# Kernel tuning notes

Hardware: AMD Instinct MI355X
Metric: run time of the kernel (lower is better)

## Reference

```python
import jax, jax.numpy as jnp
import numpy as np

N, E, D, L, H = 100000, 1600000, 64, 4, 4
C = D // H  # head dim = 16
NEG_SLOPE = 0.2


def layer_norm(x, g, b, eps=1e-5):
    m = jnp.mean(x, axis=-1, keepdims=True)
    v = jnp.var(x, axis=-1, keepdims=True)
    return (x - m) * jax.lax.rsqrt(v + eps) * g + b


def setup_inputs() -> dict:
    key = jax.random.key(0)
    ks = jax.random.split(key, 12)
    node_feats = jax.random.normal(ks[0], (N, D), jnp.float32)
    edge_feats = jax.random.normal(ks[1], (E, D), jnp.float32)
    edge_index = jax.random.randint(ks[2], (2, E), 0, N, jnp.int32)
    s = 0.1
    conv_w = jax.random.normal(ks[3], (L, D, H * C), jnp.float32) * s
    att_src = jax.random.normal(ks[4], (L, H, C), jnp.float32) * s
    att_dst = jax.random.normal(ks[5], (L, H, C), jnp.float32) * s
    edge_w = jax.random.normal(ks[6], (L, D, H * C), jnp.float32) * s
    att_edge = jax.random.normal(ks[7], (L, H, C), jnp.float32) * s
    conv_b = jnp.zeros((L, D), jnp.float32)
    ln_g = jnp.ones((L, D), jnp.float32)
    ln_b = jnp.zeros((L, D), jnp.float32)
    Din = 3 * D  # edge-update MLP input dim (node_i, node_j, edge)
    up1_w = jax.random.normal(ks[8], (L, Din, Din), jnp.float32) * 0.05
    up1_b = jnp.zeros((L, Din), jnp.float32)
    up_ln_g = jnp.ones((L, Din), jnp.float32)
    up_ln_b = jnp.zeros((L, Din), jnp.float32)
    up2_w = jax.random.normal(ks[9], (L, Din, D), jnp.float32) * 0.05
    up2_b = jnp.zeros((L, D), jnp.float32)
    return dict(node_feats=node_feats, edge_feats=edge_feats, edge_index=edge_index,
                conv_w=conv_w, att_src=att_src, att_dst=att_dst, edge_w=edge_w,
                att_edge=att_edge, conv_b=conv_b, ln_g=ln_g, ln_b=ln_b,
                up1_w=up1_w, up1_b=up1_b, up_ln_g=up_ln_g, up_ln_b=up_ln_b,
                up2_w=up2_w, up2_b=up2_b)


def _gat_conv(x, e, src, dst, w, a_s, a_d, ew, a_e, b):
    n = x.shape[0]
    # add self loops with zero edge attr
    loop = jnp.arange(n, dtype=src.dtype)
    src_f = jnp.concatenate([src, loop])
    dst_f = jnp.concatenate([dst, loop])
    xh = (x @ w).reshape(n, H, C)                       # [N,H,C]
    alpha_src = jnp.einsum('nhc,hc->nh', xh, a_s)        # [N,H]
    alpha_dst = jnp.einsum('nhc,hc->nh', xh, a_d)
    eh = (e @ ew).reshape(-1, H, C)                      # [E,H,C]
    alpha_edge = jnp.einsum('ehc,hc->eh', eh, a_e)       # [E,H]
    alpha_edge = jnp.concatenate([alpha_edge, jnp.zeros((n, H), x.dtype)])
    alpha = alpha_src[src_f] + alpha_dst[dst_f] + alpha_edge  # [E+N,H]
    alpha = jax.nn.leaky_relu(alpha, NEG_SLOPE)
    # segment softmax over destination neighborhoods
    amax = jax.ops.segment_max(alpha, dst_f, num_segments=n)
    alpha = jnp.exp(alpha - amax[dst_f])
    asum = jax.ops.segment_sum(alpha, dst_f, num_segments=n)
    alpha = alpha / (asum[dst_f] + 1e-16)
    msg = xh[src_f] * alpha[:, :, None]                  # [E+N,H,C]
    out = jax.ops.segment_sum(msg.reshape(-1, H * C), dst_f, num_segments=n)
    return out + b


def _edge_update(nf, ef, src, dst, w1, b1, g, bg, w2, b2):
    x = jnp.concatenate([nf[src], nf[dst], ef], axis=-1)  # [E,3D]
    h = layer_norm(x @ w1 + b1, g, bg)
    h = jax.nn.relu(h)
    return h @ w2 + b2 + ef


def reference(node_feats, edge_feats, edge_index, conv_w, att_src, att_dst,
              edge_w, att_edge, conv_b, ln_g, ln_b, up1_w, up1_b,
              up_ln_g, up_ln_b, up2_w, up2_b):
    src, dst = edge_index[0], edge_index[1]
    nf, ef = node_feats, edge_feats
    for l in range(L):
        conv = _gat_conv(nf, ef, src, dst, conv_w[l], att_src[l], att_dst[l],
                         edge_w[l], att_edge[l], conv_b[l])
        conv = layer_norm(conv, ln_g[l], ln_b[l])
        nf = jax.nn.relu(conv) + nf  # dropout in eval mode = identity
        ef = _edge_update(nf, ef, src, dst, up1_w[l], up1_b[l],
                          up_ln_g[l], up_ln_b[l], up2_w[l], up2_b[l])
    return nf, ef
```

## Files before the change

kernel.cpp:

```cpp
#include <hip/hip_runtime.h>
#include <math.h>

#define NN 100000
#define NE 1600000
#define DD 64
#define NL 4
#define NH 4
#define NC 16
#define DIN 192
#define SLOPE 0.2f
#define EB 64
#define XSTR 200
#define FSTR 66
#define RSTR 68
#define LOG2E 1.44269504088896340736f

typedef __bf16 bf8 __attribute__((ext_vector_type(8)));
typedef __bf16 bf4 __attribute__((ext_vector_type(4)));
typedef __bf16 bf2 __attribute__((ext_vector_type(2)));
typedef float f32x4 __attribute__((ext_vector_type(4)));

__device__ __forceinline__ f32x4 MFMA(bf8 a, bf8 b, f32x4 c) {
  return __builtin_amdgcn_mfma_f32_16x16x32_bf16(a, b, c, 0, 0, 0);
}

__global__ void k_prep(const float* __restrict__ up1_w, const float* __restrict__ up2_w,
                       const float* __restrict__ ew_all, const float* __restrict__ ae_all,
                       __bf16* __restrict__ W1H, __bf16* __restrict__ W2H,
                       float* __restrict__ vbuf, int* __restrict__ deg) {
  int bid = blockIdx.x;
  int tid = threadIdx.x;
  if (bid < 72) {
    int gidx = bid * 256 + tid;
    if (gidx >= 4 * 4608) return;
    int lyr = gidx / 4608, rem = gidx % 4608;
    int lane = rem & 63, ts = rem >> 6;
    int s = ts % 6, t = ts / 6;
    const float* Wl = up1_w + (size_t)lyr * DIN * DIN;
    size_t base = (size_t)lyr * 36864 + ((size_t)(t * 6 + s) * 64 + lane) * 8;
    int k0 = s * 32 + (lane >> 4) * 8, n = t * 16 + (lane & 15);
#pragma unroll
    for (int j = 0; j < 8; ++j)
      W1H[base + j] = (__bf16)Wl[(size_t)(k0 + j) * DIN + n];
  } else if (bid < 96) {
    int gidx = (bid - 72) * 256 + tid;
    if (gidx >= 4 * 1536) return;
    int lyr = gidx / 1536, rem = gidx % 1536;
    int lane = rem & 63, ts = rem >> 6;
    int s = ts % 6, t = ts / 6;
    const float* Wl = up2_w + (size_t)lyr * DIN * DD;
    size_t base = (size_t)lyr * 12288 + ((size_t)(t * 6 + s) * 64 + lane) * 8;
    int k0 = s * 32 + (lane >> 4) * 8, n = t * 16 + (lane & 15);
#pragma unroll
    for (int j = 0; j < 8; ++j)
      W2H[base + j] = (__bf16)Wl[(size_t)(k0 + j) * DD + n];
  } else if (bid < 100) {
    int l = bid - 96;
    const float* ew = ew_all + (size_t)l * DD * DD;
    const float* ae = ae_all + (size_t)l * NH * NC;
    int d = tid >> 2, h = tid & 3;
    float s = 0.f;
#pragma unroll
    for (int c = 0; c < NC; ++c) s = fmaf(ew[d * DD + h * NC + c], ae[h * NC + c], s);
    vbuf[l * 256 + d * NH + h] = s;
  } else {
    int i = (bid - 100) * 256 + tid;
    if (i < NN) deg[i] = 0;
  }
}

__global__ void k_w2v(const float* __restrict__ up2_w, const float* __restrict__ up2_b,
                      const float* __restrict__ vbuf, __bf16* __restrict__ W2VP,
                      __bf16* __restrict__ VP, float* __restrict__ bvdot) {
  int l = blockIdx.x;
  const float* vn = vbuf + (l + 1) * 256;
  int t = threadIdx.x;
  if (t < 384) {
    int s = t >> 6, lane = t & 63;
    int i = lane & 15, k0 = s * 32 + (lane >> 4) * 8;
    const float* W2 = up2_w + (size_t)l * DIN * DD;
    __bf16* out = W2VP + (size_t)l * 3072 + ((size_t)(s * 64 + lane)) * 8;
#pragma unroll
    for (int j = 0; j < 8; ++j) {
      float val = 0.f;
      if (i < 4)
        for (int n = 0; n < DD; ++n)
          val = fmaf(W2[(size_t)(k0 + j) * DD + n], vn[n * NH + i], val);
      out[j] = (__bf16)val;
    }
  }
  if (t < 128) {
    int s2 = t >> 6, lane = t & 63;
    int i = lane & 15, k0 = s2 * 32 + (lane >> 4) * 8;
    __bf16* out = VP + (size_t)l * 1024 + ((size_t)(s2 * 64 + lane)) * 8;
#pragma unroll
    for (int j = 0; j < 8; ++j)
      out[j] = (i < 4) ? (__bf16)vn[(k0 + j) * NH + i] : (__bf16)0.f;
  }
  if (t < 4) {
    const float* b2 = up2_b + (size_t)l * DD;
    float bv = 0.f;
    for (int n = 0; n < DD; ++n) bv = fmaf(b2[n], vn[n * NH + t], bv);
    bvdot[l * 4 + t] = bv;
  }
}

__global__ void k_hist(const int* __restrict__ dst, int* __restrict__ deg) {
  int e = blockIdx.x * 256 + threadIdx.x;
  if (e < NE) atomicAdd(&deg[dst[e]], 1);
}

__global__ void k_scan1(const int* __restrict__ deg, int* __restrict__ offs,
                        int* __restrict__ bsum) {
  __shared__ int sh[256];
  int t = threadIdx.x, b = blockIdx.x;
  int i0 = b * 1024 + t * 4;
  int d0 = (i0 + 0 < NN) ? deg[i0 + 0] : 0;
  int d1 = (i0 + 1 < NN) ? deg[i0 + 1] : 0;
  int d2 = (i0 + 2 < NN) ? deg[i0 + 2] : 0;
  int d3 = (i0 + 3 < NN) ? deg[i0 + 3] : 0;
  int s4 = d0 + d1 + d2 + d3;
  sh[t] = s4;
  __syncthreads();
  int p = 0;
#pragma unroll
  for (int off = 1; off < 256; off <<= 1) {
    int v = (t >= off) ? sh[t - off] : 0;
    __syncthreads();
    sh[t] += v;
    __syncthreads();
  }
  p = sh[t] - s4;
  if (t == 255) bsum[b] = sh[255];
  if (i0 + 0 < NN) offs[i0 + 0] = p;
  if (i0 + 1 < NN) offs[i0 + 1] = p + d0;
  if (i0 + 2 < NN) offs[i0 + 2] = p + d0 + d1;
  if (i0 + 3 < NN) offs[i0 + 3] = p + d0 + d1 + d2;
}

__global__ void k_scan2(int* __restrict__ bsum, int* __restrict__ boff,
                        int* __restrict__ offs, int nb) {
  if (threadIdx.x == 0 && blockIdx.x == 0) {
    int run = 0;
    for (int k = 0; k < nb; ++k) { boff[k] = run; run += bsum[k]; }
    offs[NN] = NE;
  }
}

__global__ void k_scan3(int* __restrict__ offs, const int* __restrict__ boff,
                        int* __restrict__ cursor) {
  int i = blockIdx.x * 256 + threadIdx.x;
  if (i < NN) {
    int v = offs[i] + boff[i >> 10];
    offs[i] = v;
    cursor[i] = v;
  }
}

__global__ void k_scatter(const int* __restrict__ src, const int* __restrict__ dst,
                          int* __restrict__ cursor, int2* __restrict__ csr_pack) {
  int e = blockIdx.x * 256 + threadIdx.x;
  if (e >= NE) return;
  int pos = atomicAdd(&cursor[dst[e]], 1);
  csr_pack[pos] = make_int2(src[e], e);
}

__global__ void k_xh0p1(const float* __restrict__ node_feats,
                        const float* __restrict__ edge_feats,
                        const float* __restrict__ W, const float* __restrict__ as_,
                        const float* __restrict__ ad_, const float* __restrict__ v,
                        __bf16* __restrict__ nf16, __bf16* __restrict__ xh16,
                        float* __restrict__ asrc, float* __restrict__ adst,
                        __bf16* __restrict__ ef16, float* __restrict__ araw) {
  int bid = blockIdx.x;
  if (bid < NN / 4 + 1) {
    int t = bid * 4 + (threadIdx.x >> 6);
    int d = threadIdx.x & 63;
    if (t >= NN) return;
    const float* x = node_feats + (size_t)t * DD;
    nf16[(size_t)t * DD + d] = (__bf16)x[d];
    float acc = 0.f;
#pragma unroll
    for (int k = 0; k < DD; ++k) acc = fmaf(x[k], W[k * DD + d], acc);
    xh16[(size_t)t * DD + d] = (__bf16)acc;
    int h = d >> 4, c = d & 15;
    float ps = acc * as_[h * NC + c];
    float pd = acc * ad_[h * NC + c];
#pragma unroll
    for (int off = 8; off >= 1; off >>= 1) {
      ps += __shfl_xor(ps, off, 64);
      pd += __shfl_xor(pd, off, 64);
    }
    if (c == 0) { asrc[t * NH + h] = ps; adst[t * NH + h] = pd; }
  } else {
    int e = (bid - (NN / 4 + 1)) * 64 + (threadIdx.x >> 2);
    int part = threadIdx.x & 3;
    if (e >= NE) return;
    float ph0 = 0.f, ph1 = 0.f, ph2 = 0.f, ph3 = 0.f;
    const float4* ep = (const float4*)(edge_feats + (size_t)e * DD + part * 16);
    const float4* v4 = (const float4*)v;
    bf4 outv[4];
#pragma unroll
    for (int c4 = 0; c4 < 4; ++c4) {
      float4 x = ep[c4];
      outv[c4][0] = (__bf16)x.x; outv[c4][1] = (__bf16)x.y;
      outv[c4][2] = (__bf16)x.z; outv[c4][3] = (__bf16)x.w;
      int d0 = part * 16 + c4 * 4;
      float4 va = v4[d0], vb = v4[d0 + 1], vc = v4[d0 + 2], vd = v4[d0 + 3];
      ph0 = fmaf(x.x, va.x, fmaf(x.y, vb.x, fmaf(x.z, vc.x, fmaf(x.w, vd.x, ph0))));
      ph1 = fmaf(x.x, va.y, fmaf(x.y, vb.y, fmaf(x.z, vc.y, fmaf(x.w, vd.y, ph1))));
      ph2 = fmaf(x.x, va.z, fmaf(x.y, vb.z, fmaf(x.z, vc.z, fmaf(x.w, vd.z, ph2))));
      ph3 = fmaf(x.x, va.w, fmaf(x.y, vb.w, fmaf(x.z, vc.w, fmaf(x.w, vd.w, ph3))));
    }
    *(bf8*)&ef16[(size_t)e * DD + part * 16] =
        (bf8){outv[0][0], outv[0][1], outv[0][2], outv[0][3],
              outv[1][0], outv[1][1], outv[1][2], outv[1][3]};
    *(bf8*)&ef16[(size_t)e * DD + part * 16 + 8] =
        (bf8){outv[2][0], outv[2][1], outv[2][2], outv[2][3],
              outv[3][0], outv[3][1], outv[3][2], outv[3][3]};
#pragma unroll
    for (int off = 1; off <= 2; off <<= 1) {
      ph0 += __shfl_xor(ph0, off, 64);
      ph1 += __shfl_xor(ph1, off, 64);
      ph2 += __shfl_xor(ph2, off, 64);
      ph3 += __shfl_xor(ph3, off, 64);
    }
    float pe = (part == 0) ? ph0 : (part == 1) ? ph1 : (part == 2) ? ph2 : ph3;
    araw[(size_t)e * NH + part] = pe;
  }
}

__global__ __launch_bounds__(256) void k_gather5(
    const __bf16* __restrict__ xh16, const float* __restrict__ araw,
    const int2* __restrict__ csr_pack, const int* __restrict__ offs,
    const float* __restrict__ asrc, const float* __restrict__ adst,
    const float* __restrict__ cb, const float* __restrict__ g,
    const float* __restrict__ bln, __bf16* __restrict__ nf16,
    float* __restrict__ nfout,
    const float* __restrict__ Wn, const float* __restrict__ asn,
    const float* __restrict__ adn, __bf16* __restrict__ xh16n,
    float* __restrict__ asrcn, float* __restrict__ adstn, int last) {
  int t = blockIdx.x * 4 + (threadIdx.x >> 6);
  int d = threadIdx.x & 63;
  if (t >= NN) return;
  int h = d >> 4;
  int o0 = offs[t], o1 = offs[t + 1];
  int deg = o1 - o0;
  float adh = adst[t * NH + h];

  float sh = asrc[t * NH + h] + adh;
  sh = ((sh > 0.f) ? sh : SLOPE * sh) * LOG2E;
  float m_run = sh;
  float wsum = 1.f;
  float acc = (float)xh16[(size_t)t * DD + d];

  int j = 0;
  for (; j + 3 < deg; j += 4) {
    int2 p0 = csr_pack[o0 + j], p1 = csr_pack[o0 + j + 1];
    int2 p2 = csr_pack[o0 + j + 2], p3 = csr_pack[o0 + j + 3];
    float ar0 = asrc[p0.x * NH + h] + adh + araw[(size_t)p0.y * NH + h];
    float ar1 = asrc[p1.x * NH + h] + adh + araw[(size_t)p1.y * NH + h];
    float ar2 = asrc[p2.x * NH + h] + adh + araw[(size_t)p2.y * NH + h];
    float ar3 = asrc[p3.x * NH + h] + adh + araw[(size_t)p3.y * NH + h];
    ar0 = ((ar0 > 0.f) ? ar0 : SLOPE * ar0) * LOG2E;
    ar1 = ((ar1 > 0.f) ? ar1 : SLOPE * ar1) * LOG2E;
    ar2 = ((ar2 > 0.f) ? ar2 : SLOPE * ar2) * LOG2E;
    ar3 = ((ar3 > 0.f) ? ar3 : SLOPE * ar3) * LOG2E;
    float x0 = (float)xh16[(size_t)p0.x * DD + d];
    float x1 = (float)xh16[(size_t)p1.x * DD + d];
    float x2 = (float)xh16[(size_t)p2.x * DD + d];
    float x3 = (float)xh16[(size_t)p3.x * DD + d];
    float mnew = fmaxf(fmaxf(m_run, fmaxf(ar0, ar1)), fmaxf(ar2, ar3));
    float rold = exp2f(m_run - mnew);
    float w0 = exp2f(ar0 - mnew), w1 = exp2f(ar1 - mnew);
    float w2 = exp2f(ar2 - mnew), w3 = exp2f(ar3 - mnew);
    acc = fmaf(w3, x3, fmaf(w2, x2, fmaf(w1, x1, fmaf(w0, x0, acc * rold))));
    wsum = (w0 + w1) + (w2 + w3) + wsum * rold;
    m_run = mnew;
  }
  for (; j < deg; ++j) {
    int2 p = csr_pack[o0 + j];
    float ar = asrc[p.x * NH + h] + adh + araw[(size_t)p.y * NH + h];
    ar = ((ar > 0.f) ? ar : SLOPE * ar) * LOG2E;
    float xv = (float)xh16[(size_t)p.x * DD + d];
    float mnew = fmaxf(m_run, ar);
    float rold = exp2f(m_run - mnew);
    float w = exp2f(ar - mnew);
    acc = fmaf(w, xv, acc * rold);
    wsum = fmaf(w, 1.f, wsum * rold);
    m_run = mnew;
  }

  float val = acc / (wsum + 1e-16f) + cb[d];
  float m = val;
#pragma unroll
  for (int off = 32; off >= 1; off >>= 1) m += __shfl_xor(m, off, 64);
  m *= (1.f / 64.f);
  float c = val - m;
  float q = c * c;
#pragma unroll
  for (int off = 32; off >= 1; off >>= 1) q += __shfl_xor(q, off, 64);
  float rstd = 1.f / sqrtf(q * (1.f / 64.f) + 1e-5f);
  float y = c * rstd * g[d] + bln[d];
  y = fmaxf(y, 0.f);
  float out = y + (float)nf16[(size_t)t * DD + d];
  nf16[(size_t)t * DD + d] = (__bf16)out;

  if (last) {
    nfout[(size_t)t * DD + d] = out;
  } else {
    float acc2 = 0.f;
#pragma unroll 8
    for (int k = 0; k < DD; ++k) {
      float xk = __shfl(out, k, 64);
      acc2 = fmaf(xk, Wn[k * DD + d], acc2);
    }
    xh16n[(size_t)t * DD + d] = (__bf16)acc2;
    int cc = d & 15;
    float ps = acc2 * asn[h * NC + cc];
    float pd = acc2 * adn[h * NC + cc];
#pragma unroll
    for (int off = 8; off >= 1; off >>= 1) {
      ps += __shfl_xor(ps, off, 64);
      pd += __shfl_xor(pd, off, 64);
    }
    if (cc == 0) { asrcn[t * NH + h] = ps; adstn[t * NH + h] = pd; }
  }
}

__global__ __launch_bounds__(256, 4) void k_edge_mlp16(
    const __bf16* __restrict__ nf16, __bf16* __restrict__ ef16,
    float* __restrict__ efout,
    const int* __restrict__ src, const int* __restrict__ dst,
    const __bf16* __restrict__ W1H, const float* __restrict__ b1,
    const float* __restrict__ g, const float* __restrict__ bg,
    const __bf16* __restrict__ W2H, const float* __restrict__ b2,
    const __bf16* __restrict__ W2VP, const __bf16* __restrict__ VP,
    const float* __restrict__ bvdot, float* __restrict__ araw, int last) {
  __shared__ __bf16 XH[EB * XSTR];
  __shared__ __bf16 RESB[EB * RSTR];
  __shared__ __bf16 Pb[EB * 8];
  int tid = threadIdx.x;
  int e0 = blockIdx.x * EB;
  float* XF = (float*)XH;

  {
    int row = tid >> 2, p = tid & 3;
    int se = src[e0 + row], de = dst[e0 + row];
    const bf8* psrc = (const bf8*)(nf16 + (size_t)se * DD + p * 16);
    *(bf8*)&XH[row * XSTR + p * 16]     = psrc[0];
    *(bf8*)&XH[row * XSTR + p * 16 + 8] = psrc[1];
    const bf8* pdst = (const bf8*)(nf16 + (size_t)de * DD + p * 16);
    *(bf8*)&XH[row * XSTR + 64 + p * 16]     = pdst[0];
    *(bf8*)&XH[row * XSTR + 64 + p * 16 + 8] = pdst[1];
    const bf8* pef = (const bf8*)(ef16 + (size_t)(e0 + row) * DD + p * 16);
    bf8 ev0 = pef[0], ev1 = pef[1];
    *(bf8*)&XH[row * XSTR + 128 + p * 16]     = ev0;
    *(bf8*)&XH[row * XSTR + 128 + p * 16 + 8] = ev1;
    *(bf8*)&RESB[row * RSTR + p * 16]     = ev0;
    *(bf8*)&RESB[row * RSTR + p * 16 + 8] = ev1;
  }
  __syncthreads();

  int cg = tid >> 6, l = tid & 63;
  int gq = l >> 4, i = l & 15;
  int col = cg * 16 + i;

  f32x4 acc[4][3];
#pragma unroll
  for (int rt = 0; rt < 4; ++rt)
#pragma unroll
    for (int t = 0; t < 3; ++t) acc[rt][t] = (f32x4){0.f, 0.f, 0.f, 0.f};
  f32x4 accQ = (f32x4){0.f, 0.f, 0.f, 0.f};

#pragma unroll
  for (int s = 0; s < 6; ++s) {
    bf8 a[4];
#pragma unroll
    for (int rt = 0; rt < 4; ++rt)
      a[rt] = *(const bf8*)&XH[(rt * 16 + i) * XSTR + s * 32 + gq * 8];
#pragma unroll
    for (int t = 0; t < 3; ++t) {
      bf8 bh = *(const bf8*)(W1H + ((size_t)((cg * 3 + t) * 6 + s) * 64 + l) * 8);
#pragma unroll
      for (int rt = 0; rt < 4; ++rt) acc[rt][t] = MFMA(a[rt], bh, acc[rt][t]);
    }
  }

  float b1v[3], gv[3], bgv[3];
#pragma unroll
  for (int t = 0; t < 3; ++t) {
    int n = cg * 48 + t * 16 + i;
    b1v[t] = b1[n]; gv[t] = g[n]; bgv[t] = bg[n];
  }
#pragma unroll
  for (int rt = 0; rt < 4; ++rt)
#pragma unroll
    for (int t = 0; t < 3; ++t)
#pragma unroll
      for (int r = 0; r < 4; ++r) acc[rt][t][r] += b1v[t];

#pragma unroll
  for (int rt = 0; rt < 4; ++rt)
#pragma unroll
    for (int r = 0; r < 4; ++r) {
      float sm = 0.f, sq = 0.f;
#pragma unroll
      for (int t = 0; t < 3; ++t) { float x = acc[rt][t][r]; sm += x; sq = fmaf(x, x, sq); }
#pragma unroll
      for (int off = 1; off <= 8; off <<= 1) {
        sm += __shfl_xor(sm, off, 64);
        sq += __shfl_xor(sq, off, 64);
      }
      if (i == 0) {
        int row = rt * 16 + gq * 4 + r;
        bf2 pr; pr[0] = (__bf16)sm; pr[1] = (__bf16)sq;
        *(bf2*)&Pb[row * 8 + cg * 2] = pr;
      }
    }
  __syncthreads();

  if (tid < EB) {
    bf8 pv = *(const bf8*)&Pb[tid * 8];
    float sm = (float)pv[0] + (float)pv[2] + (float)pv[4] + (float)pv[6];
    float sq = (float)pv[1] + (float)pv[3] + (float)pv[5] + (float)pv[7];
    float mean = sm * (1.f / (float)DIN);
    float var = sq * (1.f / (float)DIN) - mean * mean;
    float rstd = 1.f / sqrtf(var + 1e-5f);
    bf2 mv; mv[0] = (__bf16)mean; mv[1] = (__bf16)rstd;
    *(bf2*)&Pb[tid * 8] = mv;
  }
  __syncthreads();

#pragma unroll
  for (int rt = 0; rt < 4; ++rt)
#pragma unroll
    for (int r = 0; r < 4; ++r) {
      int row = rt * 16 + gq * 4 + r;
      bf2 mv = *(const bf2*)&Pb[row * 8];
      float mean = (float)mv[0], rstd = (float)mv[1];
#pragma unroll
      for (int t = 0; t < 3; ++t) {
        float y = (acc[rt][t][r] - mean) * rstd * gv[t] + bgv[t];
        y = fmaxf(y, 0.f);
        XH[row * XSTR + cg * 48 + t * 16 + i] = (__bf16)y;
      }
    }
  __syncthreads();

  f32x4 acc2[4];
#pragma unroll
  for (int rt = 0; rt < 4; ++rt) acc2[rt] = (f32x4){0.f, 0.f, 0.f, 0.f};

#pragma unroll
  for (int s = 0; s < 6; ++s) {
    bf8 a2[4];
#pragma unroll
    for (int rt = 0; rt < 4; ++rt)
      a2[rt] = *(const bf8*)&XH[(rt * 16 + i) * XSTR + s * 32 + gq * 8];
    bf8 bh = *(const bf8*)(W2H + ((size_t)(cg * 6 + s) * 64 + l) * 8);
#pragma unroll
    for (int rt = 0; rt < 4; ++rt) acc2[rt] = MFMA(a2[rt], bh, acc2[rt]);
    if (!last) {
      bf8 acg = *(const bf8*)&XH[(cg * 16 + i) * XSTR + s * 32 + gq * 8];
      bf8 wv = *(const bf8*)(W2VP + ((size_t)(s * 64 + l)) * 8);
      accQ = MFMA(acg, wv, accQ);
    }
  }
  if (!last) {
#pragma unroll
    for (int s2 = 0; s2 < 2; ++s2) {
      bf8 ae = *(const bf8*)&RESB[(cg * 16 + i) * RSTR + s2 * 32 + gq * 8];
      bf8 vp = *(const bf8*)(VP + ((size_t)(s2 * 64 + l)) * 8);
      accQ = MFMA(ae, vp, accQ);
    }
  }
  __syncthreads();

  float b2v = b2[col];
#pragma unroll
  for (int rt = 0; rt < 4; ++rt)
#pragma unroll
    for (int r = 0; r < 4; ++r) {
      int row = rt * 16 + gq * 4 + r;
      float resv = (float)RESB[row * RSTR + col];
      XF[row * FSTR + col] = acc2[rt][r] + b2v + resv;
    }

  if (!last && i < 4) {
    float bvd = bvdot[i];
#pragma unroll
    for (int r = 0; r < 4; ++r) {
      int row = cg * 16 + gq * 4 + r;
      araw[(size_t)(e0 + row) * NH + i] = accQ[r] + bvd;
    }
  }
  __syncthreads();

  {
    int row = tid >> 2, q = tid & 3;
    const float* fr = &XF[row * FSTR + q * 16];
    if (last) {
      float* op = efout + (size_t)(e0 + row) * DD + q * 16;
#pragma unroll
      for (int k = 0; k < 4; ++k)
        *(float4*)(op + k * 4) = *(const float4*)(fr + k * 4);
    } else {
      bf8 o0, o1;
#pragma unroll
      for (int k = 0; k < 8; ++k) { o0[k] = (__bf16)fr[k]; o1[k] = (__bf16)fr[k + 8]; }
      __bf16* op = ef16 + (size_t)(e0 + row) * DD + q * 16;
      *(bf8*)op = o0;
      *(bf8*)(op + 8) = o1;
    }
  }
}

extern "C" void kernel_launch(void* const* d_in, const int* in_sizes, int n_in,
                              void* d_out, int out_size, void* d_ws, size_t ws_size,
                              hipStream_t stream) {
  const float* node_feats = (const float*)d_in[0];
  const float* edge_feats = (const float*)d_in[1];
  const int*   edge_index = (const int*)d_in[2];
  const float* conv_w  = (const float*)d_in[3];
  const float* att_src = (const float*)d_in[4];
  const float* att_dst = (const float*)d_in[5];
  const float* edge_w  = (const float*)d_in[6];
  const float* att_edge= (const float*)d_in[7];
  const float* conv_b  = (const float*)d_in[8];
  const float* ln_g    = (const float*)d_in[9];
  const float* ln_b    = (const float*)d_in[10];
  const float* up1_w   = (const float*)d_in[11];
  const float* up1_b   = (const float*)d_in[12];
  const float* up_ln_g = (const float*)d_in[13];
  const float* up_ln_b = (const float*)d_in[14];
  const float* up2_w   = (const float*)d_in[15];
  const float* up2_b   = (const float*)d_in[16];

  const int* src = edge_index;
  const int* dst = edge_index + NE;

  float* nf = (float*)d_out;
  float* efout = nf + (size_t)NN * DD;

  float* w = (float*)d_ws;
  __bf16* xh16a = (__bf16*)w; w += (size_t)NN * DD / 2;
  __bf16* xh16b = (__bf16*)w; w += (size_t)NN * DD / 2;
  __bf16* nf16 = (__bf16*)w; w += (size_t)NN * DD / 2;
  __bf16* ef16 = (__bf16*)w; w += (size_t)NE * DD / 2;
  float* asA   = w; w += (size_t)NN * NH;
  float* adA   = w; w += (size_t)NN * NH;
  float* asB   = w; w += (size_t)NN * NH;
  float* adB   = w; w += (size_t)NN * NH;
  float* araw  = w; w += (size_t)NE * NH;
  float* vbuf  = w; w += 4 * 256;
  float* bvdot = w; w += 16;
  __bf16* W1H  = (__bf16*)w; w += (size_t)4 * 36864 / 2;
  __bf16* W2H  = (__bf16*)w; w += (size_t)4 * 12288 / 2;
  __bf16* W2VP = (__bf16*)w; w += (size_t)3 * 3072 / 2;
  __bf16* VPb  = (__bf16*)w; w += (size_t)3 * 1024 / 2;
  int* deg     = (int*)w; w += NN;
  int* offs    = (int*)w; w += NN + 2;
  int* cursor  = (int*)w; w += NN;
  int* bsum    = (int*)w; w += 128;
  int* boff    = (int*)w; w += 128;
  int2* csr_pack = (int2*)w; w += (size_t)NE * 2;

  __bf16* xh[2] = {xh16a, xh16b};
  float* as_[2] = {asA, asB};
  float* ad_[2] = {adA, adB};

  const int nb = (NN + 1023) / 1024;
  const int nzero = (NN + 255) / 256;

  k_prep<<<100 + nzero, 256, 0, stream>>>(up1_w, up2_w, edge_w, att_edge,
                                          W1H, W2H, vbuf, deg);
  k_hist<<<(NE + 255) / 256, 256, 0, stream>>>(dst, deg);
  k_scan1<<<nb, 256, 0, stream>>>(deg, offs, bsum);
  k_scan2<<<1, 64, 0, stream>>>(bsum, boff, offs, nb);
  k_scan3<<<(NN + 255) / 256, 256, 0, stream>>>(offs, boff, cursor);
  k_scatter<<<(NE + 255) / 256, 256, 0, stream>>>(src, dst, cursor, csr_pack);

  k_w2v<<<3, 384, 0, stream>>>(up2_w, up2_b, vbuf, W2VP, VPb, bvdot);
  k_xh0p1<<<(NN / 4 + 1) + NE / 64, 256, 0, stream>>>(
      node_feats, edge_feats, conv_w, att_src, att_dst, vbuf,
      nf16, xh16a, asA, adA, ef16, araw);

  for (int l = 0; l < NL; ++l) {
    int last = (l == NL - 1) ? 1 : 0;
    int cur = l & 1, nxt = (l + 1) & 1;
    k_gather5<<<NN / 4 + 1, 256, 0, stream>>>(
        xh[cur], araw, csr_pack, offs, as_[cur], ad_[cur],
        conv_b + (size_t)l * DD, ln_g + (size_t)l * DD, ln_b + (size_t)l * DD,
        nf16, nf,
        last ? conv_w : (conv_w + (size_t)(l + 1) * DD * DD),
        last ? att_src : (att_src + (size_t)(l + 1) * NH * NC),
        last ? att_dst : (att_dst + (size_t)(l + 1) * NH * NC),
        xh[nxt], as_[nxt], ad_[nxt], last);
    k_edge_mlp16<<<NE / EB, 256, 0, stream>>>(
        nf16, ef16, efout, src, dst,
        W1H + (size_t)l * 36864, up1_b + (size_t)l * DIN,
        up_ln_g + (size_t)l * DIN, up_ln_b + (size_t)l * DIN,
        W2H + (size_t)l * 12288, up2_b + (size_t)l * DD,
        last ? W2VP : (W2VP + (size_t)l * 3072),
        last ? VPb : (VPb + (size_t)l * 1024),
        bvdot + (size_t)l * 4, araw, last);
  }
}
```

Before: 2.524 ms.

## Store edge features and attention logits in CSR (dst-sorted) order

Edge-indexed intermediates (ef16, araw) are now stored in CSR position order instead of original edge order. The gather kernel then reads araw contiguously instead of through a random edge-id indirection. The edge MLP processes edges in dst-sorted order, so destination node reads hit cache better, and it scatters back to the original edge index only on the final-layer fp32 output. The cost is an extra csr_dst array, a permuted first read of edge_feats, and a scattered final write.

Result: no change. 2.486 ms (-1.5%).

```diff
diff --git a/kernel.cpp b/kernel.cpp
--- a/kernel.cpp
+++ b/kernel.cpp
@@ -158,17 +158,21 @@
 }
 
 __global__ void k_scatter(const int* __restrict__ src, const int* __restrict__ dst,
-                          int* __restrict__ cursor, int2* __restrict__ csr_pack) {
+                          int* __restrict__ cursor, int2* __restrict__ csr_pack,
+                          int* __restrict__ csr_dst) {
   int e = blockIdx.x * 256 + threadIdx.x;
   if (e >= NE) return;
-  int pos = atomicAdd(&cursor[dst[e]], 1);
+  int de = dst[e];
+  int pos = atomicAdd(&cursor[de], 1);
   csr_pack[pos] = make_int2(src[e], e);
+  csr_dst[pos] = de;
 }
 
 __global__ void k_xh0p1(const float* __restrict__ node_feats,
                         const float* __restrict__ edge_feats,
                         const float* __restrict__ W, const float* __restrict__ as_,
                         const float* __restrict__ ad_, const float* __restrict__ v,
+                        const int2* __restrict__ csr_pack,
                         __bf16* __restrict__ nf16, __bf16* __restrict__ xh16,
                         float* __restrict__ asrc, float* __restrict__ adst,
                         __bf16* __restrict__ ef16, float* __restrict__ araw) {
@@ -193,9 +197,10 @@
     }
     if (c == 0) { asrc[t * NH + h] = ps; adst[t * NH + h] = pd; }
   } else {
-    int e = (bid - (NN / 4 + 1)) * 64 + (threadIdx.x >> 2);
+    int pos = (bid - (NN / 4 + 1)) * 64 + (threadIdx.x >> 2);
     int part = threadIdx.x & 3;
-    if (e >= NE) return;
+    if (pos >= NE) return;
+    int e = csr_pack[pos].y;
     float ph0 = 0.f, ph1 = 0.f, ph2 = 0.f, ph3 = 0.f;
     const float4* ep = (const float4*)(edge_feats + (size_t)e * DD + part * 16);
     const float4* v4 = (const float4*)v;
@@ -212,10 +217,10 @@
       ph2 = fmaf(x.x, va.z, fmaf(x.y, vb.z, fmaf(x.z, vc.z, fmaf(x.w, vd.z, ph2))));
       ph3 = fmaf(x.x, va.w, fmaf(x.y, vb.w, fmaf(x.z, vc.w, fmaf(x.w, vd.w, ph3))));
     }
-    *(bf8*)&ef16[(size_t)e * DD + part * 16] =
+    *(bf8*)&ef16[(size_t)pos * DD + part * 16] =
         (bf8){outv[0][0], outv[0][1], outv[0][2], outv[0][3],
               outv[1][0], outv[1][1], outv[1][2], outv[1][3]};
-    *(bf8*)&ef16[(size_t)e * DD + part * 16 + 8] =
+    *(bf8*)&ef16[(size_t)pos * DD + part * 16 + 8] =
         (bf8){outv[2][0], outv[2][1], outv[2][2], outv[2][3],
               outv[3][0], outv[3][1], outv[3][2], outv[3][3]};
 #pragma unroll
@@ -226,11 +231,11 @@
       ph3 += __shfl_xor(ph3, off, 64);
     }
     float pe = (part == 0) ? ph0 : (part == 1) ? ph1 : (part == 2) ? ph2 : ph3;
-    araw[(size_t)e * NH + part] = pe;
-  }
-}
-
-__global__ __launch_bounds__(256) void k_gather5(
+    araw[(size_t)pos * NH + part] = pe;
+  }
+}
+
+__global__ __launch_bounds__(256) void k_gather7(
     const __bf16* __restrict__ xh16, const float* __restrict__ araw,
     const int2* __restrict__ csr_pack, const int* __restrict__ offs,
     const float* __restrict__ asrc, const float* __restrict__ adst,
@@ -258,10 +263,10 @@
   for (; j + 3 < deg; j += 4) {
     int2 p0 = csr_pack[o0 + j], p1 = csr_pack[o0 + j + 1];
     int2 p2 = csr_pack[o0 + j + 2], p3 = csr_pack[o0 + j + 3];
-    float ar0 = asrc[p0.x * NH + h] + adh + araw[(size_t)p0.y * NH + h];
-    float ar1 = asrc[p1.x * NH + h] + adh + araw[(size_t)p1.y * NH + h];
-    float ar2 = asrc[p2.x * NH + h] + adh + araw[(size_t)p2.y * NH + h];
-    float ar3 = asrc[p3.x * NH + h] + adh + araw[(size_t)p3.y * NH + h];
+    float ar0 = asrc[p0.x * NH + h] + adh + araw[(size_t)(o0 + j) * NH + h];
+    float ar1 = asrc[p1.x * NH + h] + adh + araw[(size_t)(o0 + j + 1) * NH + h];
+    float ar2 = asrc[p2.x * NH + h] + adh + araw[(size_t)(o0 + j + 2) * NH + h];
+    float ar3 = asrc[p3.x * NH + h] + adh + araw[(size_t)(o0 + j + 3) * NH + h];
     ar0 = ((ar0 > 0.f) ? ar0 : SLOPE * ar0) * LOG2E;
     ar1 = ((ar1 > 0.f) ? ar1 : SLOPE * ar1) * LOG2E;
     ar2 = ((ar2 > 0.f) ? ar2 : SLOPE * ar2) * LOG2E;
@@ -280,7 +285,7 @@
   }
   for (; j < deg; ++j) {
     int2 p = csr_pack[o0 + j];
-    float ar = asrc[p.x * NH + h] + adh + araw[(size_t)p.y * NH + h];
+    float ar = asrc[p.x * NH + h] + adh + araw[(size_t)(o0 + j) * NH + h];
     ar = ((ar > 0.f) ? ar : SLOPE * ar) * LOG2E;
     float xv = (float)xh16[(size_t)p.x * DD + d];
     float mnew = fmaxf(m_run, ar);
@@ -328,10 +333,10 @@
   }
 }
 
-__global__ __launch_bounds__(256, 4) void k_edge_mlp16(
+__global__ __launch_bounds__(256, 4) void k_edge_mlp18(
     const __bf16* __restrict__ nf16, __bf16* __restrict__ ef16,
     float* __restrict__ efout,
-    const int* __restrict__ src, const int* __restrict__ dst,
+    const int2* __restrict__ csr_pack, const int* __restrict__ csr_dst,
     const __bf16* __restrict__ W1H, const float* __restrict__ b1,
     const float* __restrict__ g, const float* __restrict__ bg,
     const __bf16* __restrict__ W2H, const float* __restrict__ b2,
@@ -346,7 +351,8 @@
 
   {
     int row = tid >> 2, p = tid & 3;
-    int se = src[e0 + row], de = dst[e0 + row];
+    int se = csr_pack[e0 + row].x;
+    int de = csr_dst[e0 + row];
     const bf8* psrc = (const bf8*)(nf16 + (size_t)se * DD + p * 16);
     *(bf8*)&XH[row * XSTR + p * 16]     = psrc[0];
     *(bf8*)&XH[row * XSTR + p * 16 + 8] = psrc[1];
@@ -501,7 +507,8 @@
     int row = tid >> 2, q = tid & 3;
     const float* fr = &XF[row * FSTR + q * 16];
     if (last) {
-      float* op = efout + (size_t)(e0 + row) * DD + q * 16;
+      int eout = csr_pack[e0 + row].y;
+      float* op = efout + (size_t)eout * DD + q * 16;
 #pragma unroll
       for (int k = 0; k < 4; ++k)
         *(float4*)(op + k * 4) = *(const float4*)(fr + k * 4);
@@ -564,6 +571,8 @@
   int* cursor  = (int*)w; w += NN;
   int* bsum    = (int*)w; w += 128;
   int* boff    = (int*)w; w += 128;
+  int* csr_dst = (int*)w; w += NE;
+  w += 1;
   int2* csr_pack = (int2*)w; w += (size_t)NE * 2;
 
   __bf16* xh[2] = {xh16a, xh16b};
@@ -579,17 +588,17 @@
   k_scan1<<<nb, 256, 0, stream>>>(deg, offs, bsum);
   k_scan2<<<1, 64, 0, stream>>>(bsum, boff, offs, nb);
   k_scan3<<<(NN + 255) / 256, 256, 0, stream>>>(offs, boff, cursor);
-  k_scatter<<<(NE + 255) / 256, 256, 0, stream>>>(src, dst, cursor, csr_pack);
+  k_scatter<<<(NE + 255) / 256, 256, 0, stream>>>(src, dst, cursor, csr_pack, csr_dst);
 
   k_w2v<<<3, 384, 0, stream>>>(up2_w, up2_b, vbuf, W2VP, VPb, bvdot);
   k_xh0p1<<<(NN / 4 + 1) + NE / 64, 256, 0, stream>>>(
-      node_feats, edge_feats, conv_w, att_src, att_dst, vbuf,
+      node_feats, edge_feats, conv_w, att_src, att_dst, vbuf, csr_pack,
       nf16, xh16a, asA, adA, ef16, araw);
 
   for (int l = 0; l < NL; ++l) {
     int last = (l == NL - 1) ? 1 : 0;
     int cur = l & 1, nxt = (l + 1) & 1;
-    k_gather5<<<NN / 4 + 1, 256, 0, stream>>>(
+    k_gather7<<<NN / 4 + 1, 256, 0, stream>>>(
         xh[cur], araw, csr_pack, offs, as_[cur], ad_[cur],
         conv_b + (size_t)l * DD, ln_g + (size_t)l * DD, ln_b + (size_t)l * DD,
         nf16, nf,
@@ -597,8 +606,8 @@
         last ? att_src : (att_src + (size_t)(l + 1) * NH * NC),
         last ? att_dst : (att_dst + (size_t)(l + 1) * NH * NC),
         xh[nxt], as_[nxt], ad_[nxt], last);
-    k_edge_mlp16<<<NE / EB, 256, 0, stream>>>(
-        nf16, ef16, efout, src, dst,
+    k_edge_mlp18<<<NE / EB, 256, 0, stream>>>(
+        nf16, ef16, efout, csr_pack, csr_dst,
         W1H + (size_t)l * 36864, up1_b + (size_t)l * DIN,
         up_ln_g + (size_t)l * DIN, up_ln_b + (size_t)l * DIN,
         W2H + (size_t)l * 12288, up2_b + (size_t)l * DD,
```
